# Performance work log

Measured on AMD Instinct MI355X. Metric: run time of the kernel, lower is better.

Reference implementation:

```python
import jax, jax.numpy as jnp
import numpy as np

C = 256
K = 8
CQK = C // K  # 32 query/key channels


def setup_inputs() -> dict:
    key = jax.random.key(0)
    ks = jax.random.split(key, 10)
    B, H, W = 8, 64, 64
    s = 0.02
    return {
        "x": jax.random.normal(ks[0], (B, C, H, W), jnp.float32),
        "Wf": jax.random.normal(ks[1], (CQK, C), jnp.float32) * s,
        "bf": jax.random.normal(ks[2], (CQK,), jnp.float32) * s,
        "Wg": jax.random.normal(ks[3], (CQK, C), jnp.float32) * s,
        "bg": jax.random.normal(ks[4], (CQK,), jnp.float32) * s,
        "Wh": jax.random.normal(ks[5], (C, C), jnp.float32) * s,
        "bh": jax.random.normal(ks[6], (C,), jnp.float32) * s,
        "Wv": jax.random.normal(ks[7], (C, C), jnp.float32) * s,
        "bv": jax.random.normal(ks[8], (C,), jnp.float32) * s,
        "gamma": jax.random.normal(ks[9], (1,), jnp.float32) * 0.1,
    }


def _conv1x1(x, W, b):
    # x: [B,C,H,W], W: [O,C] -> [B,O,H,W]
    return jnp.einsum("oc,bchw->bohw", W, x) + b[None, :, None, None]


def reference(x, Wf, bf, Wg, bg, Wh, bh, Wv, bv, gamma):
    B, Cc, Hd, Wd = x.shape
    N = Hd * Wd
    f = _conv1x1(x, Wf, bf).reshape(B, CQK, N)   # keys of query i
    g = _conv1x1(x, Wg, bg).reshape(B, CQK, N)
    h = _conv1x1(x, Wh, bh).reshape(B, Cc, N)
    # att[b,i,j] = softmax_j( f_i . g_j )
    att = jnp.einsum("bci,bcj->bij", f, g)       # [B,N,N]
    att = jax.nn.softmax(att, axis=-1)
    # out[b,c,i] = sum_j h[b,c,j] * att[b,i,j]
    att_h = jnp.einsum("bcj,bij->bci", h, att).reshape(B, Cc, Hd, Wd)
    att_h = _conv1x1(att_h, Wv, bv)
    return x + gamma[0] * att_h
```

## Files before the change

### kernel.cpp

```cpp
#include <hip/hip_runtime.h>
#include <hip/hip_bf16.h>
#include <stdint.h>

#define BATCH 8
#define CH    256
#define CQK   32
#define NPIX  4096
#define MALL  320

using bfrag = __attribute__((ext_vector_type(8))) short;
using f32x4 = __attribute__((ext_vector_type(4))) float;
using u32x2 = __attribute__((ext_vector_type(2))) unsigned int;

#define MFMA16(A, B, C) __builtin_amdgcn_mfma_f32_16x16x32_bf16(A, B, C, 0, 0, 0)

__device__ __forceinline__ unsigned short f2bf(float f) {
  union { float f; unsigned int u; } v; v.f = f;
  unsigned int r = v.u + 0x7FFFu + ((v.u >> 16) & 1u);
  return (unsigned short)(r >> 16);
}

__device__ __forceinline__ void gload_lds16(const void* g, void* l) {
  __builtin_amdgcn_global_load_lds(
      (const __attribute__((address_space(1))) unsigned int*)g,
      (__attribute__((address_space(3))) unsigned int*)l, 16, 0, 0);
}

__global__ void prep_kernel(const float* __restrict__ Wf, const float* __restrict__ Wg,
                            const float* __restrict__ Wh, const float* __restrict__ Wv,
                            unsigned short* __restrict__ Wall, unsigned short* __restrict__ Wvb) {
  int i = blockIdx.x * 256 + threadIdx.x;
  if (i < MALL * CH) {
    int m = i >> 8, c = i & 255;
    float v = (m < CQK)     ? Wf[m * CH + c]
            : (m < 2 * CQK) ? Wg[(m - CQK) * CH + c]
                            : Wh[(m - 2 * CQK) * CH + c];
    Wall[i] = f2bf(v);
  }
  if (i < CH * CH) Wvb[i] = f2bf(Wv[i]);
}

__global__ __launch_bounds__(256, 2)
void proj_kernel(const float* __restrict__ x, const unsigned short* __restrict__ Wall,
                 const float* __restrict__ bfb, const float* __restrict__ bgb,
                 const float* __restrict__ bhb,
                 unsigned short* __restrict__ Qo, unsigned short* __restrict__ Ko,
                 unsigned short* __restrict__ Vo) {
  __shared__ char xT[64 * 512];
  const int b  = blockIdx.x & 7;
  const int n0 = (blockIdx.x >> 3) * 64;
  const int tid = threadIdx.x;
  const int lane = tid & 63, wave = tid >> 6;
  const int lr = lane & 15, g = lane >> 4;

  for (int it = 0; it < 16; ++it) {
    int c = it * 16 + wave * 4 + g;
    int nn = lr * 4;
    const float4 v = *(const float4*)(x + (size_t)(b * CH + c) * NPIX + n0 + nn);
    const float* vp = (const float*)&v;
#pragma unroll
    for (int j = 0; j < 4; ++j) {
      int n = nn + j;
      int byteoff = n * 512 + (((c >> 3) ^ (n & 7)) << 4) + ((c & 7) * 2);
      *(unsigned short*)(xT + byteoff) = f2bf(vp[j]);
    }
  }
  __syncthreads();

  f32x4 acc[5][4] = {};
  for (int ks = 0; ks < 8; ++ks) {
    bfrag bfr[4];
#pragma unroll
    for (int nt = 0; nt < 4; ++nt) {
      int n = nt * 16 + lr;
      bfr[nt] = *(const bfrag*)(xT + n * 512 + (((ks * 4 + g) ^ (n & 7)) << 4));
    }
#pragma unroll
    for (int i = 0; i < 5; ++i) {
      int m = (wave + 4 * i) * 16 + lr;
      bfrag afr = *(const bfrag*)(Wall + (size_t)m * CH + ks * 32 + g * 8);
#pragma unroll
      for (int nt = 0; nt < 4; ++nt) acc[i][nt] = MFMA16(afr, bfr[nt], acc[i][nt]);
    }
  }

#pragma unroll
  for (int i = 0; i < 5; ++i) {
    const int mt = wave + 4 * i;
#pragma unroll
    for (int nt = 0; nt < 4; ++nt) {
      const int n = n0 + nt * 16 + lr;
      if (mt < 2) {
        float v0 = acc[i][nt][0] + bfb[mt * 16 + 4 * g + 0];
        float v1 = acc[i][nt][1] + bfb[mt * 16 + 4 * g + 1];
        float v2 = acc[i][nt][2] + bfb[mt * 16 + 4 * g + 2];
        float v3 = acc[i][nt][3] + bfb[mt * 16 + 4 * g + 3];
        u32x2 pk;
        pk[0] = (unsigned)f2bf(v0) | ((unsigned)f2bf(v1) << 16);
        pk[1] = (unsigned)f2bf(v2) | ((unsigned)f2bf(v3) << 16);
        *(u32x2*)(Qo + (size_t)(b * NPIX + n) * CQK + mt * 16 + 4 * g) = pk;
      } else if (mt < 4) {
        int k0 = (mt - 2) * 16 + 4 * g;
        float v0 = acc[i][nt][0] + bgb[k0 + 0];
        float v1 = acc[i][nt][1] + bgb[k0 + 1];
        float v2 = acc[i][nt][2] + bgb[k0 + 2];
        float v3 = acc[i][nt][3] + bgb[k0 + 3];
        u32x2 pk;
        pk[0] = (unsigned)f2bf(v0) | ((unsigned)f2bf(v1) << 16);
        pk[1] = (unsigned)f2bf(v2) | ((unsigned)f2bf(v3) << 16);
        *(u32x2*)(Ko + (size_t)(b * NPIX + n) * CQK + k0) = pk;
      } else {
#pragma unroll
        for (int r = 0; r < 4; ++r) {
          int c = mt * 16 + 4 * g + r - 64;
          Vo[(size_t)(b * CH + c) * NPIX + n] = f2bf(acc[i][nt][r] + bhb[c]);
        }
      }
    }
  }
}

__global__ __launch_bounds__(256, 2)
void attn_kernel(const unsigned short* __restrict__ Qg, const unsigned short* __restrict__ Kg,
                 const unsigned short* __restrict__ Vg, unsigned short* __restrict__ Og) {
  extern __shared__ char smem[];
  char* const Kb0 = smem;
  char* const Kb1 = smem + 4096;
  char* const Vb0 = smem + 8192;
  char* const Vb1 = smem + 8192 + 32768;
  char* const Pb  = smem + 8192 + 65536;

  const int b  = blockIdx.x & 7;
  const int q0 = (blockIdx.x >> 3) * 64;
  const int tid = threadIdx.x;
  const int lane = tid & 63, wave = tid >> 6;
  const int lr = lane & 15, g = lane >> 4;

  const unsigned short* Qbase = Qg + (size_t)(b * NPIX + q0) * CQK;
  const unsigned short* Kbase = Kg + (size_t)b * NPIX * CQK;
  const unsigned short* Vbase = Vg + (size_t)b * CH * NPIX;

  bfrag qf[4];
#pragma unroll
  for (int nt = 0; nt < 4; ++nt)
    qf[nt] = *(const bfrag*)(Qbase + (nt * 16 + lr) * CQK + g * 8);

  const unsigned short* vsrc[8];
#pragma unroll
  for (int i = 0; i < 8; ++i) {
    int ch = i * 256 + tid;
    int c = ch >> 3, G = ch & 7;
    vsrc[i] = Vbase + (size_t)c * NPIX + (G ^ (c & 7)) * 8;
  }
  const unsigned short* ksrc;
  {
    int row = tid >> 2, G = tid & 3;
    ksrc = Kbase + (size_t)row * CQK + (G ^ ((row ^ (row >> 2)) & 3)) * 8;
  }

  auto stage = [&](int t, char* kb, char* vb) {
    gload_lds16(ksrc + (size_t)t * 64 * CQK, kb + wave * 1024);
#pragma unroll
    for (int i = 0; i < 8; ++i)
      gload_lds16(vsrc[i] + (size_t)t * 64, vb + (i * 256 + wave * 64) * 16);
  };

  f32x4 acc[4][4] = {};
  float lp[4] = {0.f, 0.f, 0.f, 0.f};

  const int krow = 16 * wave + lr;
  const int koff = krow * 64 + ((g ^ ((krow ^ (krow >> 2)) & 3)) << 4);
  const int pwG  = 2 * wave + (g >> 1);

  stage(0, Kb0, Vb0);
  __syncthreads();

  for (int t = 0; t < 64; ++t) {
    char* kb  = (t & 1) ? Kb1 : Kb0;
    char* vb  = (t & 1) ? Vb1 : Vb0;
    char* kbn = (t & 1) ? Kb0 : Kb1;
    char* vbn = (t & 1) ? Vb0 : Vb1;

    bfrag kf = *(const bfrag*)(kb + koff);
#pragma unroll
    for (int nt = 0; nt < 4; ++nt) {
      f32x4 zero = 0.0f;
      f32x4 st = MFMA16(kf, qf[nt], zero);
      float p0 = __expf(st[0]), p1 = __expf(st[1]);
      float p2 = __expf(st[2]), p3 = __expf(st[3]);
      lp[nt] += (p0 + p1) + (p2 + p3);
      int q = nt * 16 + lr;
      u32x2 pk;
      pk[0] = (unsigned)f2bf(p0) | ((unsigned)f2bf(p1) << 16);
      pk[1] = (unsigned)f2bf(p2) | ((unsigned)f2bf(p3) << 16);
      *(u32x2*)(Pb + q * 128 + ((pwG ^ (q & 7)) << 4) + ((g & 1) << 3)) = pk;
    }
    __syncthreads();

    if (t + 1 < 64) stage(t + 1, kbn, vbn);

#pragma unroll
    for (int ks = 0; ks < 2; ++ks) {
      bfrag pf[4], vf[4];
#pragma unroll
      for (int mt = 0; mt < 4; ++mt) {
        int q = mt * 16 + lr;
        pf[mt] = *(const bfrag*)(Pb + q * 128 + (((ks * 4 + g) ^ (q & 7)) << 4));
      }
#pragma unroll
      for (int nt = 0; nt < 4; ++nt) {
        int c = 64 * wave + nt * 16 + lr;
        vf[nt] = *(const bfrag*)(vb + c * 128 + (((ks * 4 + g) ^ (c & 7)) << 4));
      }
#pragma unroll
      for (int mt = 0; mt < 4; ++mt)
#pragma unroll
        for (int nt = 0; nt < 4; ++nt)
          acc[mt][nt] = MFMA16(pf[mt], vf[nt], acc[mt][nt]);
    }
    __syncthreads();
  }

#pragma unroll
  for (int nt = 0; nt < 4; ++nt) {
    lp[nt] += __shfl_xor(lp[nt], 16);
    lp[nt] += __shfl_xor(lp[nt], 32);
  }
  float* lred = (float*)Pb;
  if (lane < 16) {
#pragma unroll
    for (int nt = 0; nt < 4; ++nt) lred[wave * 64 + nt * 16 + lr] = lp[nt];
  }
  __syncthreads();
  float inv[4][4];
#pragma unroll
  for (int mt = 0; mt < 4; ++mt)
#pragma unroll
    for (int r = 0; r < 4; ++r) {
      int q = mt * 16 + 4 * g + r;
      float s = lred[q] + lred[64 + q] + lred[128 + q] + lred[192 + q];
      inv[mt][r] = 1.0f / s;
    }
#pragma unroll
  for (int mt = 0; mt < 4; ++mt)
#pragma unroll
    for (int nt = 0; nt < 4; ++nt) {
      int c = 64 * wave + nt * 16 + lr;
#pragma unroll
      for (int r = 0; r < 4; ++r) {
        int q = q0 + mt * 16 + 4 * g + r;
        Og[(size_t)(b * NPIX + q) * CH + c] = f2bf(acc[mt][nt][r] * inv[mt][r]);
      }
    }
}

__global__ __launch_bounds__(256, 2)
void vproj_kernel(const unsigned short* __restrict__ attn, const unsigned short* __restrict__ Wvb,
                  const float* __restrict__ bv, const float* __restrict__ x,
                  const float* __restrict__ gamma, float* __restrict__ out) {
  __shared__ char at[64 * 512];
  const int b  = blockIdx.x & 7;
  const int n0 = (blockIdx.x >> 3) * 64;
  const int tid = threadIdx.x;
  const int lane = tid & 63, wave = tid >> 6;
  const int lr = lane & 15, g = lane >> 4;

#pragma unroll
  for (int i = 0; i < 8; ++i) {
    int ch = i * 256 + tid;
    int n = ch >> 5, G = ch & 31;
    gload_lds16(attn + (size_t)(b * NPIX + n0 + n) * CH + (G ^ (n & 7)) * 8,
                at + (i * 256 + wave * 64) * 16);
  }
  __syncthreads();

  f32x4 acc[4][4] = {};
  for (int ks = 0; ks < 8; ++ks) {
    bfrag bfr[4];
#pragma unroll
    for (int nt = 0; nt < 4; ++nt) {
      int n = nt * 16 + lr;
      bfr[nt] = *(const bfrag*)(at + n * 512 + (((ks * 4 + g) ^ (n & 7)) << 4));
    }
#pragma unroll
    for (int i = 0; i < 4; ++i) {
      int m = (wave * 4 + i) * 16 + lr;
      bfrag afr = *(const bfrag*)(Wvb + (size_t)m * CH + ks * 32 + g * 8);
#pragma unroll
      for (int nt = 0; nt < 4; ++nt) acc[i][nt] = MFMA16(afr, bfr[nt], acc[i][nt]);
    }
  }
  const float gam = gamma[0];
#pragma unroll
  for (int i = 0; i < 4; ++i)
#pragma unroll
    for (int nt = 0; nt < 4; ++nt) {
      int n = n0 + nt * 16 + lr;
#pragma unroll
      for (int r = 0; r < 4; ++r) {
        int m = (wave * 4 + i) * 16 + 4 * g + r;
        size_t off = (size_t)(b * CH + m) * NPIX + n;
        out[off] = x[off] + gam * (acc[i][nt][r] + bv[m]);
      }
    }
}

extern "C" void kernel_launch(void* const* d_in, const int* in_sizes, int n_in,
                              void* d_out, int out_size, void* d_ws, size_t ws_size,
                              hipStream_t stream) {
  const float* x   = (const float*)d_in[0];
  const float* Wf  = (const float*)d_in[1];
  const float* bfb = (const float*)d_in[2];
  const float* Wg  = (const float*)d_in[3];
  const float* bgb = (const float*)d_in[4];
  const float* Wh  = (const float*)d_in[5];
  const float* bhb = (const float*)d_in[6];
  const float* Wv  = (const float*)d_in[7];
  const float* bv  = (const float*)d_in[8];
  const float* gam = (const float*)d_in[9];
  float* out = (float*)d_out;

  char* ws = (char*)d_ws;
  unsigned short* Wall = (unsigned short*)(ws);
  unsigned short* Wvb  = (unsigned short*)(ws + 163840);
  unsigned short* Q    = (unsigned short*)(ws + 294912);
  unsigned short* K    = (unsigned short*)(ws + 2392064);
  unsigned short* V    = (unsigned short*)(ws + 4489216);
  unsigned short* attn = (unsigned short*)(ws + 21266432);

  (void)hipFuncSetAttribute((const void*)attn_kernel,
                            hipFuncAttributeMaxDynamicSharedMemorySize, 81920);

  prep_kernel<<<320, 256, 0, stream>>>(Wf, Wg, Wh, Wv, Wall, Wvb);
  proj_kernel<<<512, 256, 0, stream>>>(x, Wall, bfb, bgb, bhb, Q, K, V);
  attn_kernel<<<512, 256, 81920, stream>>>(Q, K, V, attn);
  vproj_kernel<<<512, 256, 0, stream>>>(attn, Wvb, bv, x, gam, out);
}
```

Baseline: 140.9 us.

## Load K/V fragments directly from global into registers, dropping LDS staging

The attention kernel no longer double-buffers K and V tiles in LDS via global_load_lds. Each wave now reads its K and V MFMA fragments straight from global memory into registers, and only the P tile stays in shared memory. LDS use drops from 80KB to 8KB, which could allow more blocks per CU. The exponent is switched to exp2 with log2(e) folded into Q during projection, and bf16 packing uses cheaper rounding. The cost is strided, uncoalesced V global loads with latency that is only partly hidden, and more register pressure.

Result: slower. 176.0 us (+24.9%).

```diff
diff --git a/kernel.cpp b/kernel.cpp
--- a/kernel.cpp
+++ b/kernel.cpp
@@ -13,6 +13,12 @@
 using u32x2 = __attribute__((ext_vector_type(2))) unsigned int;
 
 #define MFMA16(A, B, C) __builtin_amdgcn_mfma_f32_16x16x32_bf16(A, B, C, 0, 0, 0)
+
+#if __has_builtin(__builtin_amdgcn_exp2f)
+#define EXP2(x) __builtin_amdgcn_exp2f(x)
+#else
+#define EXP2(x) exp2f(x)
+#endif
 
 __device__ __forceinline__ unsigned short f2bf(float f) {
   union { float f; unsigned int u; } v; v.f = f;
@@ -84,6 +90,7 @@
     }
   }
 
+  const float L2E = 1.4426950408889634f;
 #pragma unroll
   for (int i = 0; i < 5; ++i) {
     const int mt = wave + 4 * i;
@@ -91,10 +98,10 @@
     for (int nt = 0; nt < 4; ++nt) {
       const int n = n0 + nt * 16 + lr;
       if (mt < 2) {
-        float v0 = acc[i][nt][0] + bfb[mt * 16 + 4 * g + 0];
-        float v1 = acc[i][nt][1] + bfb[mt * 16 + 4 * g + 1];
-        float v2 = acc[i][nt][2] + bfb[mt * 16 + 4 * g + 2];
-        float v3 = acc[i][nt][3] + bfb[mt * 16 + 4 * g + 3];
+        float v0 = (acc[i][nt][0] + bfb[mt * 16 + 4 * g + 0]) * L2E;
+        float v1 = (acc[i][nt][1] + bfb[mt * 16 + 4 * g + 1]) * L2E;
+        float v2 = (acc[i][nt][2] + bfb[mt * 16 + 4 * g + 2]) * L2E;
+        float v3 = (acc[i][nt][3] + bfb[mt * 16 + 4 * g + 3]) * L2E;
         u32x2 pk;
         pk[0] = (unsigned)f2bf(v0) | ((unsigned)f2bf(v1) << 16);
         pk[1] = (unsigned)f2bf(v2) | ((unsigned)f2bf(v3) << 16);
@@ -120,15 +127,10 @@
   }
 }
 
-__global__ __launch_bounds__(256, 2)
+__global__ __launch_bounds__(256)
 void attn_kernel(const unsigned short* __restrict__ Qg, const unsigned short* __restrict__ Kg,
                  const unsigned short* __restrict__ Vg, unsigned short* __restrict__ Og) {
-  extern __shared__ char smem[];
-  char* const Kb0 = smem;
-  char* const Kb1 = smem + 4096;
-  char* const Vb0 = smem + 8192;
-  char* const Vb1 = smem + 8192 + 32768;
-  char* const Pb  = smem + 8192 + 65536;
+  __shared__ char Pb[8192];
 
   const int b  = blockIdx.x & 7;
   const int q0 = (blockIdx.x >> 3) * 64;
@@ -137,88 +139,67 @@
   const int lr = lane & 15, g = lane >> 4;
 
   const unsigned short* Qbase = Qg + (size_t)(b * NPIX + q0) * CQK;
-  const unsigned short* Kbase = Kg + (size_t)b * NPIX * CQK;
-  const unsigned short* Vbase = Vg + (size_t)b * CH * NPIX;
+  const unsigned short* Kfp   = Kg + (size_t)b * NPIX * CQK + (size_t)(16 * wave + lr) * CQK + g * 8;
+  const unsigned short* Vfp   = Vg + (size_t)b * CH * NPIX + g * 8;
 
   bfrag qf[4];
 #pragma unroll
   for (int nt = 0; nt < 4; ++nt)
     qf[nt] = *(const bfrag*)(Qbase + (nt * 16 + lr) * CQK + g * 8);
 
-  const unsigned short* vsrc[8];
-#pragma unroll
-  for (int i = 0; i < 8; ++i) {
-    int ch = i * 256 + tid;
-    int c = ch >> 3, G = ch & 7;
-    vsrc[i] = Vbase + (size_t)c * NPIX + (G ^ (c & 7)) * 8;
-  }
-  const unsigned short* ksrc;
-  {
-    int row = tid >> 2, G = tid & 3;
-    ksrc = Kbase + (size_t)row * CQK + (G ^ ((row ^ (row >> 2)) & 3)) * 8;
-  }
-
-  auto stage = [&](int t, char* kb, char* vb) {
-    gload_lds16(ksrc + (size_t)t * 64 * CQK, kb + wave * 1024);
-#pragma unroll
-    for (int i = 0; i < 8; ++i)
-      gload_lds16(vsrc[i] + (size_t)t * 64, vb + (i * 256 + wave * 64) * 16);
-  };
-
   f32x4 acc[4][4] = {};
   float lp[4] = {0.f, 0.f, 0.f, 0.f};
-
-  const int krow = 16 * wave + lr;
-  const int koff = krow * 64 + ((g ^ ((krow ^ (krow >> 2)) & 3)) << 4);
-  const int pwG  = 2 * wave + (g >> 1);
-
-  stage(0, Kb0, Vb0);
-  __syncthreads();
+  const int pwG = 2 * wave + (g >> 1);
+
+  bfrag kf = *(const bfrag*)(Kfp);
 
   for (int t = 0; t < 64; ++t) {
-    char* kb  = (t & 1) ? Kb1 : Kb0;
-    char* vb  = (t & 1) ? Vb1 : Vb0;
-    char* kbn = (t & 1) ? Kb0 : Kb1;
-    char* vbn = (t & 1) ? Vb0 : Vb1;
-
-    bfrag kf = *(const bfrag*)(kb + koff);
-#pragma unroll
-    for (int nt = 0; nt < 4; ++nt) {
-      f32x4 zero = 0.0f;
+    bfrag vf[2][4];
+#pragma unroll
+    for (int ks = 0; ks < 2; ++ks)
+#pragma unroll
+      for (int nt = 0; nt < 4; ++nt)
+        vf[ks][nt] = *(const bfrag*)(Vfp + (size_t)(64 * wave + nt * 16 + lr) * NPIX
+                                         + t * 64 + ks * 32);
+
+#pragma unroll
+    for (int nt = 0; nt < 4; ++nt) {
+      f32x4 zero = {0.f, 0.f, 0.f, 0.f};
       f32x4 st = MFMA16(kf, qf[nt], zero);
-      float p0 = __expf(st[0]), p1 = __expf(st[1]);
-      float p2 = __expf(st[2]), p3 = __expf(st[3]);
+      float p0 = EXP2(st[0]), p1 = EXP2(st[1]);
+      float p2 = EXP2(st[2]), p3 = EXP2(st[3]);
       lp[nt] += (p0 + p1) + (p2 + p3);
+      union { float f; unsigned u; } u0, u1, u2, u3;
+      u0.f = p0; u1.f = p1; u2.f = p2; u3.f = p3;
+      u32x2 pk;
+      pk[0] = ((u0.u + 0x8000u) >> 16) | ((u1.u + 0x8000u) & 0xFFFF0000u);
+      pk[1] = ((u2.u + 0x8000u) >> 16) | ((u3.u + 0x8000u) & 0xFFFF0000u);
       int q = nt * 16 + lr;
-      u32x2 pk;
-      pk[0] = (unsigned)f2bf(p0) | ((unsigned)f2bf(p1) << 16);
-      pk[1] = (unsigned)f2bf(p2) | ((unsigned)f2bf(p3) << 16);
       *(u32x2*)(Pb + q * 128 + ((pwG ^ (q & 7)) << 4) + ((g & 1) << 3)) = pk;
     }
-    __syncthreads();
-
-    if (t + 1 < 64) stage(t + 1, kbn, vbn);
+
+    kf = *(const bfrag*)(Kfp + (size_t)(((t + 1) & 63) * 64) * CQK);
+
+    asm volatile("s_waitcnt lgkmcnt(0)" ::: "memory");
+    __builtin_amdgcn_s_barrier();
 
 #pragma unroll
     for (int ks = 0; ks < 2; ++ks) {
-      bfrag pf[4], vf[4];
+      bfrag pf[4];
 #pragma unroll
       for (int mt = 0; mt < 4; ++mt) {
         int q = mt * 16 + lr;
         pf[mt] = *(const bfrag*)(Pb + q * 128 + (((ks * 4 + g) ^ (q & 7)) << 4));
       }
 #pragma unroll
-      for (int nt = 0; nt < 4; ++nt) {
-        int c = 64 * wave + nt * 16 + lr;
-        vf[nt] = *(const bfrag*)(vb + c * 128 + (((ks * 4 + g) ^ (c & 7)) << 4));
-      }
-#pragma unroll
       for (int mt = 0; mt < 4; ++mt)
 #pragma unroll
         for (int nt = 0; nt < 4; ++nt)
-          acc[mt][nt] = MFMA16(pf[mt], vf[nt], acc[mt][nt]);
-    }
-    __syncthreads();
+          acc[mt][nt] = MFMA16(pf[mt], vf[ks][nt], acc[mt][nt]);
+    }
+
+    asm volatile("s_waitcnt lgkmcnt(0)" ::: "memory");
+    __builtin_amdgcn_s_barrier();
   }
 
 #pragma unroll
@@ -328,11 +309,8 @@
   unsigned short* V    = (unsigned short*)(ws + 4489216);
   unsigned short* attn = (unsigned short*)(ws + 21266432);
 
-  (void)hipFuncSetAttribute((const void*)attn_kernel,
-                            hipFuncAttributeMaxDynamicSharedMemorySize, 81920);
-
   prep_kernel<<<320, 256, 0, stream>>>(Wf, Wg, Wh, Wv, Wall, Wvb);
   proj_kernel<<<512, 256, 0, stream>>>(x, Wall, bfb, bgb, bhb, Q, K, V);
-  attn_kernel<<<512, 256, 81920, stream>>>(Q, K, V, attn);
+  attn_kernel<<<512, 256, 0, stream>>>(Q, K, V, attn);
   vproj_kernel<<<512, 256, 0, stream>>>(attn, Wvb, bv, x, gam, out);
 }
```
